# Kernel optimization log

Hardware: AMD Instinct MI355X
Metric: run time of the kernel (lower is better)

The kernel has to match this reference:

```python
import jax, jax.numpy as jnp
import numpy as np

EMBED = 1024

def setup_inputs() -> dict:
    key = jax.random.key(0)
    ks = jax.random.split(key, 7)
    s = 1.0 / np.sqrt(EMBED)
    x = jax.random.normal(ks[0], (8, 2048, EMBED), dtype=jnp.float32)
    Wk = jax.random.uniform(ks[1], (EMBED, EMBED), jnp.float32, -s, s)
    bk = jax.random.uniform(ks[2], (EMBED,), jnp.float32, -s, s)
    Wq = jax.random.uniform(ks[3], (EMBED, EMBED), jnp.float32, -s, s)
    bq = jax.random.uniform(ks[4], (EMBED,), jnp.float32, -s, s)
    Wv = jax.random.uniform(ks[5], (EMBED, EMBED), jnp.float32, -s, s)
    bv = jax.random.uniform(ks[6], (EMBED,), jnp.float32, -s, s)
    return {"x": x, "Wq": Wq, "bq": bq, "Wk": Wk, "bk": bk, "Wv": Wv, "bv": bv}

def reference(x, Wq, bq, Wk, bk, Wv, bv):
    # Linear projections (PyTorch Linear: y = x @ W^T + b; W here stored as [in, out] = W^T)
    Q = x @ Wq + bq          # [b, s, d]
    K = x @ Wk + bk
    V = x @ Wv + bv
    scale = 1.0 / jnp.sqrt(jnp.asarray(x.shape[-1], x.dtype))
    scores = jnp.einsum('bqd,bkd->bqk', Q, K) * scale  # [b, s, s]
    attn = jax.nn.softmax(scores, axis=-1)
    return jnp.einsum('bqk,bkd->bqd', attn, V)
```

## Files before the change

kernel.cpp:

```cpp
#include <hip/hip_runtime.h>

typedef __attribute__((ext_vector_type(4))) float f32x4;
typedef __attribute__((ext_vector_type(8))) short bf16x8;
typedef __attribute__((ext_vector_type(4))) unsigned short u16x4;

static __device__ __forceinline__ unsigned short f2bf(float f) {
    union { float f; unsigned int u; } a; a.f = f;
    unsigned int u = a.u;
    unsigned int r = (u + 0x7FFFu + ((u >> 16) & 1u)) >> 16;
    return (unsigned short)r;
}
static __device__ __forceinline__ float bf2f(unsigned short h) {
    union { unsigned int u; float f; } a; a.u = ((unsigned int)h) << 16;
    return a.f;
}
static __device__ __forceinline__ unsigned lds_off(const void* p) {
    return (unsigned)(unsigned long long)(const __attribute__((address_space(3))) void*)p;
}

__global__ __launch_bounds__(256) void cvt_f32_bf16(const float* __restrict__ in,
                                                    unsigned short* __restrict__ out) {
    long long i = ((long long)blockIdx.x * 256 + threadIdx.x) * 4;
    float4 f = *(const float4*)(in + i);
    u16x4 u;
    u[0] = f2bf(f.x); u[1] = f2bf(f.y); u[2] = f2bf(f.z); u[3] = f2bf(f.w);
    *(u16x4*)(out + i) = u;
}

__global__ __launch_bounds__(256) void transpose_w(const float* __restrict__ W0,
                                                   const float* __restrict__ W1,
                                                   const float* __restrict__ W2,
                                                   unsigned short* __restrict__ Wt) {
    __shared__ float t[32][33];
    int mat = blockIdx.z;
    const float* W = (mat == 0) ? W0 : (mat == 1) ? W1 : W2;
    unsigned short* out = Wt + (long long)mat * 1024 * 1024;
    int n0 = blockIdx.x * 32, k0 = blockIdx.y * 32;
    int tx = threadIdx.x, ty = threadIdx.y;
#pragma unroll
    for (int q = 0; q < 4; ++q)
        t[ty + 8 * q][tx] = W[(long long)(k0 + ty + 8 * q) * 1024 + n0 + tx];
    __syncthreads();
#pragma unroll
    for (int q = 0; q < 4; ++q)
        out[(long long)(n0 + ty + 8 * q) * 1024 + k0 + tx] = f2bf(t[tx][ty + 8 * q]);
}

#define GBM 256
#define GBN 256

template<int OUT_MODE, int BIAS_MODE>
__global__ __launch_bounds__(512, 2) void gemmcv(
    const unsigned short* __restrict__ A, int lda, long long strideA,
    const unsigned short* __restrict__ B, int ldb, long long strideB,
    void* __restrict__ Cv, int ldc, long long strideC,
    const float* __restrict__ bias, int K, float scale)
{
    __shared__ __align__(16) char lds[131072];

    const int gx = gridDim.x, gy = gridDim.y;
    int lin = blockIdx.x + gx * (blockIdx.y + gy * blockIdx.z);
    const int nwg = gx * gy * gridDim.z;
    const int qch = nwg >> 3;
    int swz = (lin & 7) * qch + (lin >> 3);
    const int bx = swz % gx; int t2 = swz / gx;
    const int by = t2 % gy;  const int bz = t2 / gy;

    const unsigned short* Ag = A + (long long)bz * strideA;
    const unsigned short* Bg = B + (long long)bz * strideB;
    const int m0 = by * GBM, n0 = bx * GBN;

    const int tid  = threadIdx.x;
    const int lane = tid & 63, w = tid >> 6;
    const int wm = w >> 2, wn = w & 3;
    const int l15 = lane & 15, l4 = lane >> 4;

    const int sr = lane >> 3;
    const int ss = (lane & 7) ^ sr;
    const unsigned short* Asrc = Ag + (long long)(m0 + w * 8 + sr) * lda + ss * 8;
    const unsigned short* Bsrc = Bg + (long long)(n0 + w * 8 + sr) * ldb + ss * 8;

    f32x4 acc[8][4] = {};

    auto stageA = [&](int p, int kt, int h) {
#pragma unroll
        for (int i = 0; i < 2; ++i)
            __builtin_amdgcn_global_load_lds(
                (const __attribute__((address_space(1))) void*)(Asrc + (long long)(h * 128 + i * 64) * lda + kt),
                (__attribute__((address_space(3))) void*)(lds + p * 32768 + (h * 128 + i * 64 + w * 8) * 128), 16, 0, 0);
    };
    auto stageB = [&](int p, int kt, int h) {
#pragma unroll
        for (int i = 0; i < 2; ++i)
            __builtin_amdgcn_global_load_lds(
                (const __attribute__((address_space(1))) void*)(Bsrc + (long long)(h * 128 + i * 64) * ldb + kt),
                (__attribute__((address_space(3))) void*)(lds + 65536 + p * 32768 + (h * 128 + i * 64 + w * 8) * 128), 16, 0, 0);
    };

    const unsigned ldsb = lds_off(lds);
    const unsigned as0  = (unsigned)(((l4    ) ^ (l15 & 7)) * 16);
    const unsigned as1  = (unsigned)(((l4 + 4) ^ (l15 & 7)) * 16);
    const unsigned aRow = (unsigned)((wm * 128 + l15) * 128);
    const unsigned bRow = (unsigned)((wn * 64 + l15) * 128);

    bf16x8 aA[4], aB[4], aC[4], aD[4], bA[4], bB[4];
    auto readA = [&](bf16x8 (&af)[4], int p, int mh, int ks) {
        unsigned base = ldsb + (unsigned)(p * 32768) + aRow + (unsigned)(mh * 8192) + (ks ? as1 : as0);
#pragma unroll
        for (int fi = 0; fi < 4; ++fi) {
            unsigned off = base + (unsigned)(fi * 2048);
            asm volatile("ds_read_b128 %0, %1" : "=v"(af[fi]) : "v"(off));
        }
    };
    auto readB = [&](bf16x8 (&bf)[4], int p, int ks) {
        unsigned base = ldsb + 65536u + (unsigned)(p * 32768) + bRow + (ks ? as1 : as0);
#pragma unroll
        for (int nj = 0; nj < 4; ++nj) {
            unsigned off = base + (unsigned)(nj * 2048);
            asm volatile("ds_read_b128 %0, %1" : "=v"(bf[nj]) : "v"(off));
        }
    };
    auto mfma16 = [&](int mh, bf16x8 (&af)[4], bf16x8 (&bf)[4]) {
#pragma unroll
        for (int fi = 0; fi < 4; ++fi)
#pragma unroll
            for (int nj = 0; nj < 4; ++nj)
                acc[mh * 4 + fi][nj] = __builtin_amdgcn_mfma_f32_16x16x32_bf16(
                    af[fi], bf[nj], acc[mh * 4 + fi][nj], 0, 0, 0);
    };

#define VMCNT4 asm volatile("s_waitcnt vmcnt(4)" ::: "memory")
#define VMCNT2 asm volatile("s_waitcnt vmcnt(2)" ::: "memory")
#define VMCNT0 asm volatile("s_waitcnt vmcnt(0)" ::: "memory")
#define LGKM8  asm volatile("s_waitcnt lgkmcnt(8)" ::: "memory")
#define LGKM4  asm volatile("s_waitcnt lgkmcnt(4)" ::: "memory")
#define LGKM0  asm volatile("s_waitcnt lgkmcnt(0)" ::: "memory")
#define SCHED0 __builtin_amdgcn_sched_barrier(0)
#define BARR   __builtin_amdgcn_s_barrier()
#define PRIO1  __builtin_amdgcn_s_setprio(1)
#define PRIO0  __builtin_amdgcn_s_setprio(0)

    const int NT = K >> 6;
    stageB(0, 0, 0); stageB(0, 0, 1); stageA(0, 0, 0); stageA(0, 0, 1);

    for (int t = 0; t < NT; ++t) {
        const int p = t & 1, q = p ^ 1;
        const int kt1 = (t + 1) << 6;
        const bool s1 = (t + 1) < NT;
        VMCNT2; BARR; SCHED0;
        if (s1) { stageB(q, kt1, 0); stageB(q, kt1, 1); }
        readA(aA, p, 0, 0); readB(bA, p, 0);
        readA(aC, p, 0, 1); readB(bB, p, 1);
        LGKM8; SCHED0; PRIO1; mfma16(0, aA, bA); PRIO0;
        if (s1) { VMCNT4; } else { VMCNT0; }
        BARR; SCHED0;
        if (s1) { stageA(q, kt1, 0); stageA(q, kt1, 1); }
        readA(aB, p, 1, 0); readA(aD, p, 1, 1);
        LGKM8; SCHED0; PRIO1; mfma16(0, aC, bB); PRIO0;
        LGKM4; SCHED0; PRIO1; mfma16(1, aB, bA); PRIO0;
        LGKM0; SCHED0; PRIO1; mfma16(1, aD, bB); PRIO0;
    }

    const float* bias_v = bias;
    asm volatile("" : "+s"(bias_v));
    unsigned short* Cb = (unsigned short*)Cv;
    float* Cf = (float*)Cv;
    long long cbase = (long long)bz * strideC;
#pragma unroll
    for (int mh = 0; mh < 2; ++mh)
#pragma unroll
    for (int fi = 0; fi < 4; ++fi) {
#pragma unroll
        for (int nj = 0; nj < 4; ++nj) {
            int n = n0 + wn * 64 + nj * 16 + l15;
            float bn = (BIAS_MODE == 1) ? bias_v[n] : 0.0f;
#pragma unroll
            for (int r = 0; r < 4; ++r) {
                int m = m0 + wm * 128 + mh * 64 + fi * 16 + l4 * 4 + r;
                float v = acc[mh * 4 + fi][nj][r] * scale + bn;
                if (BIAS_MODE == 2) v += bias_v[m];
                long long idx = cbase + (long long)m * ldc + n;
                if (OUT_MODE == 0) Cb[idx] = f2bf(v);
                else               Cf[idx] = v;
            }
        }
    }
}

__global__ __launch_bounds__(256) void softmax_rows_bf16(unsigned short* __restrict__ S) {
    int row  = blockIdx.x * 4 + (threadIdx.x >> 6);
    int lane = threadIdx.x & 63;
    unsigned short* Srow = S + (long long)row * 2048;
    float v[32];
    float mx = -1e30f;
#pragma unroll
    for (int j = 0; j < 4; ++j) {
        bf16x8 h = *(const bf16x8*)(Srow + j * 512 + lane * 8);
#pragma unroll
        for (int e = 0; e < 8; ++e) {
            float f = bf2f((unsigned short)h[e]);
            v[j * 8 + e] = f;
            mx = fmaxf(mx, f);
        }
    }
#pragma unroll
    for (int o = 32; o; o >>= 1) mx = fmaxf(mx, __shfl_xor(mx, o));
    float sum = 0.0f;
#pragma unroll
    for (int e = 0; e < 32; ++e) {
        v[e] = __expf(v[e] - mx);
        sum += v[e];
    }
#pragma unroll
    for (int o = 32; o; o >>= 1) sum += __shfl_xor(sum, o);
    float inv = 1.0f / sum;
#pragma unroll
    for (int j = 0; j < 4; ++j) {
        bf16x8 h;
#pragma unroll
        for (int e = 0; e < 8; ++e) h[e] = (short)f2bf(v[j * 8 + e] * inv);
        *(bf16x8*)(Srow + j * 512 + lane * 8) = h;
    }
}

extern "C" void kernel_launch(void* const* d_in, const int* in_sizes, int n_in,
                              void* d_out, int out_size, void* d_ws, size_t ws_size,
                              hipStream_t stream) {
    (void)in_sizes; (void)n_in; (void)out_size; (void)ws_size;
    const float* x  = (const float*)d_in[0];
    const float* Wq = (const float*)d_in[1];
    const float* bq = (const float*)d_in[2];
    const float* Wk = (const float*)d_in[3];
    const float* bk = (const float*)d_in[4];
    const float* Wv = (const float*)d_in[5];
    const float* bv = (const float*)d_in[6];

    char* ws = (char*)d_ws;
    unsigned short* Wt  = (unsigned short*)ws;
    unsigned short* Qb  = (unsigned short*)(ws + 6291456);
    unsigned short* Kb  = (unsigned short*)(ws + 39845888);
    unsigned short* Vt  = (unsigned short*)(ws + 73400320);
    unsigned short* xb  = (unsigned short*)(ws + 106954752);
    unsigned short* Sb  = (unsigned short*)(ws + 106954752);

    cvt_f32_bf16<<<dim3(16384), dim3(256), 0, stream>>>(x, xb);
    transpose_w<<<dim3(32, 32, 3), dim3(32, 8), 0, stream>>>(Wq, Wk, Wv, Wt);

    gemmcv<0, 1><<<dim3(4, 64, 1), dim3(512), 0, stream>>>(
        xb, 1024, 0, Wt, 1024, 0, Qb, 1024, 0, bq, 1024, 1.0f);
    gemmcv<0, 1><<<dim3(4, 64, 1), dim3(512), 0, stream>>>(
        xb, 1024, 0, Wt + 1048576, 1024, 0, Kb, 1024, 0, bk, 1024, 1.0f);
    gemmcv<0, 2><<<dim3(64, 4, 1), dim3(512), 0, stream>>>(
        Wt + 2097152, 1024, 0, xb, 1024, 0, Vt, 16384, 0, bv, 1024, 1.0f);

    gemmcv<0, 0><<<dim3(8, 8, 8), dim3(512), 0, stream>>>(
        Qb, 1024, 2097152LL, Kb, 1024, 2097152LL,
        Sb, 2048, 4194304LL, nullptr, 1024, 0.03125f);

    softmax_rows_bf16<<<dim3(4096), dim3(256), 0, stream>>>(Sb);

    gemmcv<1, 0><<<dim3(4, 8, 8), dim3(512), 0, stream>>>(
        Sb, 2048, 4194304LL,
        Vt, 16384, 2048LL,
        d_out, 1024, 2097152LL, nullptr, 2048, 1.0f);
}
```

Baseline: 278.0 us.

## Stage A tile through registers instead of direct global-to-LDS loads

The A operand is now loaded from global memory into registers early in each iteration and written to the alternate LDS buffer late, while B keeps using direct global_load_lds. This removes the mid-iteration barrier and vmcnt wait that gated the A staging, leaving one barrier per K step. In exchange it uses extra VGPRs for the staged A fragments and adds explicit ds_write traffic that competes with the ds_reads used by the MFMAs.

After: 300.8 us. +8.2%, slower.

```diff
diff --git a/kernel.cpp b/kernel.cpp
--- a/kernel.cpp
+++ b/kernel.cpp
@@ -50,7 +50,7 @@
 #define GBN 256
 
 template<int OUT_MODE, int BIAS_MODE>
-__global__ __launch_bounds__(512, 2) void gemmcv(
+__global__ __launch_bounds__(512, 2) void gemmt14(
     const unsigned short* __restrict__ A, int lda, long long strideA,
     const unsigned short* __restrict__ B, int ldb, long long strideB,
     void* __restrict__ Cv, int ldc, long long strideC,
@@ -80,15 +80,17 @@
     const unsigned short* Asrc = Ag + (long long)(m0 + w * 8 + sr) * lda + ss * 8;
     const unsigned short* Bsrc = Bg + (long long)(n0 + w * 8 + sr) * ldb + ss * 8;
 
+    const unsigned short* AsrcJ[4];
+    unsigned awr[4];
+#pragma unroll
+    for (int j = 0; j < 4; ++j) {
+        AsrcJ[j] = Asrc + (long long)(j * 64) * lda;
+        awr[j]   = (unsigned)((j * 64 + w * 8 + sr) * 128 + (lane & 7) * 16);
+    }
+    bf16x8 areg[4];
+
     f32x4 acc[8][4] = {};
 
-    auto stageA = [&](int p, int kt, int h) {
-#pragma unroll
-        for (int i = 0; i < 2; ++i)
-            __builtin_amdgcn_global_load_lds(
-                (const __attribute__((address_space(1))) void*)(Asrc + (long long)(h * 128 + i * 64) * lda + kt),
-                (__attribute__((address_space(3))) void*)(lds + p * 32768 + (h * 128 + i * 64 + w * 8) * 128), 16, 0, 0);
-    };
     auto stageB = [&](int p, int kt, int h) {
 #pragma unroll
         for (int i = 0; i < 2; ++i)
@@ -129,8 +131,6 @@
                     af[fi], bf[nj], acc[mh * 4 + fi][nj], 0, 0, 0);
     };
 
-#define VMCNT4 asm volatile("s_waitcnt vmcnt(4)" ::: "memory")
-#define VMCNT2 asm volatile("s_waitcnt vmcnt(2)" ::: "memory")
 #define VMCNT0 asm volatile("s_waitcnt vmcnt(0)" ::: "memory")
 #define LGKM8  asm volatile("s_waitcnt lgkmcnt(8)" ::: "memory")
 #define LGKM4  asm volatile("s_waitcnt lgkmcnt(4)" ::: "memory")
@@ -141,24 +141,35 @@
 #define PRIO0  __builtin_amdgcn_s_setprio(0)
 
     const int NT = K >> 6;
-    stageB(0, 0, 0); stageB(0, 0, 1); stageA(0, 0, 0); stageA(0, 0, 1);
+#pragma unroll
+    for (int j = 0; j < 4; ++j) areg[j] = *(const bf16x8*)(AsrcJ[j]);
+    stageB(0, 0, 0); stageB(0, 0, 1);
+#pragma unroll
+    for (int j = 0; j < 4; ++j) *(bf16x8*)(&lds[awr[j]]) = areg[j];
+    LGKM0; VMCNT0; BARR; SCHED0;
 
     for (int t = 0; t < NT; ++t) {
         const int p = t & 1, q = p ^ 1;
         const int kt1 = (t + 1) << 6;
         const bool s1 = (t + 1) < NT;
-        VMCNT2; BARR; SCHED0;
-        if (s1) { stageB(q, kt1, 0); stageB(q, kt1, 1); }
+        if (s1) {
+#pragma unroll
+            for (int j = 0; j < 4; ++j) areg[j] = *(const bf16x8*)(AsrcJ[j] + kt1);
+            stageB(q, kt1, 0); stageB(q, kt1, 1);
+        }
         readA(aA, p, 0, 0); readB(bA, p, 0);
         readA(aC, p, 0, 1); readB(bB, p, 1);
         LGKM8; SCHED0; PRIO1; mfma16(0, aA, bA); PRIO0;
-        if (s1) { VMCNT4; } else { VMCNT0; }
-        BARR; SCHED0;
-        if (s1) { stageA(q, kt1, 0); stageA(q, kt1, 1); }
         readA(aB, p, 1, 0); readA(aD, p, 1, 1);
         LGKM8; SCHED0; PRIO1; mfma16(0, aC, bB); PRIO0;
         LGKM4; SCHED0; PRIO1; mfma16(1, aB, bA); PRIO0;
+        if (s1) {
+#pragma unroll
+            for (int j = 0; j < 4; ++j) *(bf16x8*)(&lds[(q * 32768) + awr[j]]) = areg[j];
+        }
         LGKM0; SCHED0; PRIO1; mfma16(1, aD, bB); PRIO0;
+        if (s1) { VMCNT0; }
+        BARR; SCHED0;
     }
 
     const float* bias_v = bias;
@@ -246,20 +257,20 @@
     cvt_f32_bf16<<<dim3(16384), dim3(256), 0, stream>>>(x, xb);
     transpose_w<<<dim3(32, 32, 3), dim3(32, 8), 0, stream>>>(Wq, Wk, Wv, Wt);
 
-    gemmcv<0, 1><<<dim3(4, 64, 1), dim3(512), 0, stream>>>(
+    gemmt14<0, 1><<<dim3(4, 64, 1), dim3(512), 0, stream>>>(
         xb, 1024, 0, Wt, 1024, 0, Qb, 1024, 0, bq, 1024, 1.0f);
-    gemmcv<0, 1><<<dim3(4, 64, 1), dim3(512), 0, stream>>>(
+    gemmt14<0, 1><<<dim3(4, 64, 1), dim3(512), 0, stream>>>(
         xb, 1024, 0, Wt + 1048576, 1024, 0, Kb, 1024, 0, bk, 1024, 1.0f);
-    gemmcv<0, 2><<<dim3(64, 4, 1), dim3(512), 0, stream>>>(
+    gemmt14<0, 2><<<dim3(64, 4, 1), dim3(512), 0, stream>>>(
         Wt + 2097152, 1024, 0, xb, 1024, 0, Vt, 16384, 0, bv, 1024, 1.0f);
 
-    gemmcv<0, 0><<<dim3(8, 8, 8), dim3(512), 0, stream>>>(
+    gemmt14<0, 0><<<dim3(8, 8, 8), dim3(512), 0, stream>>>(
         Qb, 1024, 2097152LL, Kb, 1024, 2097152LL,
         Sb, 2048, 4194304LL, nullptr, 1024, 0.03125f);
 
     softmax_rows_bf16<<<dim3(4096), dim3(256), 0, stream>>>(Sb);
 
-    gemmcv<1, 0><<<dim3(4, 8, 8), dim3(512), 0, stream>>>(
+    gemmt14<1, 0><<<dim3(4, 8, 8), dim3(512), 0, stream>>>(
         Sb, 2048, 4194304LL,
         Vt, 16384, 2048LL,
         d_out, 1024, 2097152LL, nullptr, 2048, 1.0f);
```

## Store Q and K in FP8 and compute attention scores with FP8 MFMA

Applied to the files above, without the earlier changes.

The Q and K projection GEMMs now write FP8 e4m3 outputs pre-scaled by 16 instead of bf16. A new FP8 GEMM kernel computes QK^T with 16x16x32 fp8 MFMA over 128-wide K tiles, with new LDS swizzling and a reworked read/compute schedule, then rescales the result into bf16 scores. This halves Q/K memory traffic and raises matrix throughput for the score GEMM, at the cost of lower precision in the attention scores.

New measurement: 270.9 us. 1.03x faster.

```diff
diff --git a/kernel.cpp b/kernel.cpp
--- a/kernel.cpp
+++ b/kernel.cpp
@@ -1,4 +1,5 @@
 #include <hip/hip_runtime.h>
+#include <hip/hip_fp8.h>
 
 typedef __attribute__((ext_vector_type(4))) float f32x4;
 typedef __attribute__((ext_vector_type(8))) short bf16x8;
@@ -13,6 +14,10 @@
 static __device__ __forceinline__ float bf2f(unsigned short h) {
     union { unsigned int u; float f; } a; a.u = ((unsigned int)h) << 16;
     return a.f;
+}
+static __device__ __forceinline__ unsigned char f2fp8(float f) {
+    __hip_fp8_e4m3 h(f);
+    return *reinterpret_cast<const unsigned char*>(&h);
 }
 static __device__ __forceinline__ unsigned lds_off(const void* p) {
     return (unsigned)(unsigned long long)(const __attribute__((address_space(3))) void*)p;
@@ -46,6 +51,18 @@
         out[(long long)(n0 + ty + 8 * q) * 1024 + k0 + tx] = f2bf(t[tx][ty + 8 * q]);
 }
 
+#define SCHED0 __builtin_amdgcn_sched_barrier(0)
+#define BARR   __builtin_amdgcn_s_barrier()
+#define PRIO1  __builtin_amdgcn_s_setprio(1)
+#define PRIO0  __builtin_amdgcn_s_setprio(0)
+#define VMCNT4 asm volatile("s_waitcnt vmcnt(4)" ::: "memory")
+#define VMCNT2 asm volatile("s_waitcnt vmcnt(2)" ::: "memory")
+#define VMCNT0 asm volatile("s_waitcnt vmcnt(0)" ::: "memory")
+#define LGKM12 asm volatile("s_waitcnt lgkmcnt(12)" ::: "memory")
+#define LGKM8  asm volatile("s_waitcnt lgkmcnt(8)" ::: "memory")
+#define LGKM4  asm volatile("s_waitcnt lgkmcnt(4)" ::: "memory")
+#define LGKM0  asm volatile("s_waitcnt lgkmcnt(0)" ::: "memory")
+
 #define GBM 256
 #define GBN 256
 
@@ -128,17 +145,6 @@
                 acc[mh * 4 + fi][nj] = __builtin_amdgcn_mfma_f32_16x16x32_bf16(
                     af[fi], bf[nj], acc[mh * 4 + fi][nj], 0, 0, 0);
     };
-
-#define VMCNT4 asm volatile("s_waitcnt vmcnt(4)" ::: "memory")
-#define VMCNT2 asm volatile("s_waitcnt vmcnt(2)" ::: "memory")
-#define VMCNT0 asm volatile("s_waitcnt vmcnt(0)" ::: "memory")
-#define LGKM8  asm volatile("s_waitcnt lgkmcnt(8)" ::: "memory")
-#define LGKM4  asm volatile("s_waitcnt lgkmcnt(4)" ::: "memory")
-#define LGKM0  asm volatile("s_waitcnt lgkmcnt(0)" ::: "memory")
-#define SCHED0 __builtin_amdgcn_sched_barrier(0)
-#define BARR   __builtin_amdgcn_s_barrier()
-#define PRIO1  __builtin_amdgcn_s_setprio(1)
-#define PRIO0  __builtin_amdgcn_s_setprio(0)
 
     const int NT = K >> 6;
     stageB(0, 0, 0); stageB(0, 0, 1); stageA(0, 0, 0); stageA(0, 0, 1);
@@ -164,6 +170,7 @@
     const float* bias_v = bias;
     asm volatile("" : "+s"(bias_v));
     unsigned short* Cb = (unsigned short*)Cv;
+    unsigned char*  C8 = (unsigned char*)Cv;
     float* Cf = (float*)Cv;
     long long cbase = (long long)bz * strideC;
 #pragma unroll
@@ -180,8 +187,136 @@
                 float v = acc[mh * 4 + fi][nj][r] * scale + bn;
                 if (BIAS_MODE == 2) v += bias_v[m];
                 long long idx = cbase + (long long)m * ldc + n;
-                if (OUT_MODE == 0) Cb[idx] = f2bf(v);
-                else               Cf[idx] = v;
+                if (OUT_MODE == 0)      Cb[idx] = f2bf(v);
+                else if (OUT_MODE == 1) Cf[idx] = v;
+                else                    C8[idx] = f2fp8(v * 16.0f);
+            }
+        }
+    }
+}
+
+__global__ __launch_bounds__(512, 2) void gemmf8(
+    const unsigned char* __restrict__ A, int lda, long long strideA,
+    const unsigned char* __restrict__ B, int ldb, long long strideB,
+    unsigned short* __restrict__ C, int ldc, long long strideC,
+    int K, float scale)
+{
+    __shared__ __align__(16) char lds[131072];
+
+    const int gx = gridDim.x, gy = gridDim.y;
+    int lin = blockIdx.x + gx * (blockIdx.y + gy * blockIdx.z);
+    const int nwg = gx * gy * gridDim.z;
+    const int qch = nwg >> 3;
+    int swz = (lin & 7) * qch + (lin >> 3);
+    const int bx = swz % gx; int t2 = swz / gx;
+    const int by = t2 % gy;  const int bz = t2 / gy;
+
+    const unsigned char* Ag = A + (long long)bz * strideA;
+    const unsigned char* Bg = B + (long long)bz * strideB;
+    const int m0 = by * GBM, n0 = bx * GBN;
+
+    const int tid  = threadIdx.x;
+    const int lane = tid & 63, w = tid >> 6;
+    const int wm = w >> 2, wn = w & 3;
+    const int l15 = lane & 15, l4 = lane >> 4;
+
+    const int sr = lane >> 3;
+    const int c7 = lane & 7;
+    const int ss8 = (((((c7 >> 1) ^ (sr & 3)) << 1) | ((c7 & 1) ^ ((lane >> 5) & 1)))) * 16;
+    const unsigned char* Asrc = Ag + (long long)(m0 + w * 8 + sr) * lda + ss8;
+    const unsigned char* Bsrc = Bg + (long long)(n0 + w * 8 + sr) * ldb + ss8;
+
+    f32x4 acc[8][4] = {};
+
+    auto stageA = [&](int p, int kt, int h) {
+#pragma unroll
+        for (int i = 0; i < 2; ++i)
+            __builtin_amdgcn_global_load_lds(
+                (const __attribute__((address_space(1))) void*)(Asrc + (long long)(h * 128 + i * 64) * lda + kt),
+                (__attribute__((address_space(3))) void*)(lds + p * 32768 + (h * 128 + i * 64 + w * 8) * 128), 16, 0, 0);
+    };
+    auto stageB = [&](int p, int kt, int h) {
+#pragma unroll
+        for (int i = 0; i < 2; ++i)
+            __builtin_amdgcn_global_load_lds(
+                (const __attribute__((address_space(1))) void*)(Bsrc + (long long)(h * 128 + i * 64) * ldb + kt),
+                (__attribute__((address_space(3))) void*)(lds + 65536 + p * 32768 + (h * 128 + i * 64 + w * 8) * 128), 16, 0, 0);
+    };
+
+    const unsigned ldsb  = lds_off(lds);
+    const unsigned kbase = (unsigned)((l4 << 3) ^ (((l15 >> 2) & 1) << 4));
+    unsigned kk[4];
+#pragma unroll
+    for (int ks = 0; ks < 4; ++ks) kk[ks] = (unsigned)((ks ^ (l15 & 3)) << 5) + kbase;
+    const unsigned aRow = (unsigned)((wm * 128 + l15) * 128);
+    const unsigned bRow = (unsigned)((wn * 64 + l15) * 128) + 65536u;
+
+    long a0[4][4], a1[4][4], bb[4][4];
+    auto readA = [&](long (&af)[4], int p, int mh, int ks) {
+        unsigned base = ldsb + (unsigned)(p * 32768) + aRow + (unsigned)(mh * 8192) + kk[ks];
+#pragma unroll
+        for (int fi = 0; fi < 4; ++fi) {
+            unsigned off = base + (unsigned)(fi * 2048);
+            asm volatile("ds_read_b64 %0, %1" : "=v"(af[fi]) : "v"(off));
+        }
+    };
+    auto readB = [&](long (&bf)[4], int p, int ks) {
+        unsigned base = ldsb + (unsigned)(p * 32768) + bRow + kk[ks];
+#pragma unroll
+        for (int nj = 0; nj < 4; ++nj) {
+            unsigned off = base + (unsigned)(nj * 2048);
+            asm volatile("ds_read_b64 %0, %1" : "=v"(bf[nj]) : "v"(off));
+        }
+    };
+    auto mf = [&](int mh, long (&af)[4], long (&bf)[4]) {
+#pragma unroll
+        for (int fi = 0; fi < 4; ++fi)
+#pragma unroll
+            for (int nj = 0; nj < 4; ++nj)
+                acc[mh * 4 + fi][nj] = __builtin_amdgcn_mfma_f32_16x16x32_fp8_fp8(
+                    af[fi], bf[nj], acc[mh * 4 + fi][nj], 0, 0, 0);
+    };
+
+    const int NT = K >> 7;
+    stageB(0, 0, 0); stageB(0, 0, 1); stageA(0, 0, 0); stageA(0, 0, 1);
+
+    for (int t = 0; t < NT; ++t) {
+        const int p = t & 1, q = p ^ 1;
+        const int kt1 = (t + 1) << 7;
+        const bool s1 = (t + 1) < NT;
+        VMCNT2; BARR; SCHED0;
+        if (s1) { stageB(q, kt1, 0); stageB(q, kt1, 1); }
+        readA(a0[0], p, 0, 0); readB(bb[0], p, 0);
+        readA(a0[1], p, 0, 1); readB(bb[1], p, 1);
+        LGKM8; SCHED0; PRIO1; mf(0, a0[0], bb[0]); PRIO0;
+        readA(a0[2], p, 0, 2); readB(bb[2], p, 2);
+        LGKM8; SCHED0; PRIO1; mf(0, a0[1], bb[1]); PRIO0;
+        if (s1) { VMCNT4; } else { VMCNT0; }
+        BARR; SCHED0;
+        if (s1) { stageA(q, kt1, 0); stageA(q, kt1, 1); }
+        readA(a0[3], p, 0, 3); readB(bb[3], p, 3);
+        LGKM8; SCHED0; PRIO1; mf(0, a0[2], bb[2]); PRIO0;
+        readA(a1[0], p, 1, 0); readA(a1[1], p, 1, 1);
+        LGKM8; SCHED0; PRIO1; mf(0, a0[3], bb[3]); PRIO0;
+        readA(a1[2], p, 1, 2); readA(a1[3], p, 1, 3);
+        LGKM12; SCHED0; PRIO1; mf(1, a1[0], bb[0]); PRIO0;
+        LGKM8;  SCHED0; PRIO1; mf(1, a1[1], bb[1]); PRIO0;
+        LGKM4;  SCHED0; PRIO1; mf(1, a1[2], bb[2]); PRIO0;
+        LGKM0;  SCHED0; PRIO1; mf(1, a1[3], bb[3]); PRIO0;
+    }
+
+    long long cbase = (long long)bz * strideC;
+#pragma unroll
+    for (int mh = 0; mh < 2; ++mh)
+#pragma unroll
+    for (int fi = 0; fi < 4; ++fi) {
+#pragma unroll
+        for (int nj = 0; nj < 4; ++nj) {
+            int n = n0 + wn * 64 + nj * 16 + l15;
+#pragma unroll
+            for (int r = 0; r < 4; ++r) {
+                int m = m0 + wm * 128 + mh * 64 + fi * 16 + l4 * 4 + r;
+                C[cbase + (long long)m * ldc + n] = f2bf(acc[mh * 4 + fi][nj][r] * scale);
             }
         }
     }
@@ -237,25 +372,25 @@
 
     char* ws = (char*)d_ws;
     unsigned short* Wt  = (unsigned short*)ws;
-    unsigned short* Qb  = (unsigned short*)(ws + 6291456);
-    unsigned short* Kb  = (unsigned short*)(ws + 39845888);
-    unsigned short* Vt  = (unsigned short*)(ws + 73400320);
-    unsigned short* xb  = (unsigned short*)(ws + 106954752);
-    unsigned short* Sb  = (unsigned short*)(ws + 106954752);
+    unsigned char*  Qb8 = (unsigned char*) (ws + 6291456);
+    unsigned char*  Kb8 = (unsigned char*) (ws + 23068672);
+    unsigned short* Vt  = (unsigned short*)(ws + 39845888);
+    unsigned short* xb  = (unsigned short*)(ws + 73400320);
+    unsigned short* Sb  = (unsigned short*)(ws + 73400320);
 
     cvt_f32_bf16<<<dim3(16384), dim3(256), 0, stream>>>(x, xb);
     transpose_w<<<dim3(32, 32, 3), dim3(32, 8), 0, stream>>>(Wq, Wk, Wv, Wt);
 
-    gemmcv<0, 1><<<dim3(4, 64, 1), dim3(512), 0, stream>>>(
-        xb, 1024, 0, Wt, 1024, 0, Qb, 1024, 0, bq, 1024, 1.0f);
-    gemmcv<0, 1><<<dim3(4, 64, 1), dim3(512), 0, stream>>>(
-        xb, 1024, 0, Wt + 1048576, 1024, 0, Kb, 1024, 0, bk, 1024, 1.0f);
+    gemmcv<2, 1><<<dim3(4, 64, 1), dim3(512), 0, stream>>>(
+        xb, 1024, 0, Wt, 1024, 0, Qb8, 1024, 0, bq, 1024, 1.0f);
+    gemmcv<2, 1><<<dim3(4, 64, 1), dim3(512), 0, stream>>>(
+        xb, 1024, 0, Wt + 1048576, 1024, 0, Kb8, 1024, 0, bk, 1024, 1.0f);
     gemmcv<0, 2><<<dim3(64, 4, 1), dim3(512), 0, stream>>>(
         Wt + 2097152, 1024, 0, xb, 1024, 0, Vt, 16384, 0, bv, 1024, 1.0f);
 
-    gemmcv<0, 0><<<dim3(8, 8, 8), dim3(512), 0, stream>>>(
-        Qb, 1024, 2097152LL, Kb, 1024, 2097152LL,
-        Sb, 2048, 4194304LL, nullptr, 1024, 0.03125f);
+    gemmf8<<<dim3(8, 8, 8), dim3(512), 0, stream>>>(
+        Qb8, 1024, 2097152LL, Kb8, 1024, 2097152LL,
+        Sb, 2048, 4194304LL, 1024, 1.0f / 8192.0f);
 
     softmax_rows_bf16<<<dim3(4096), dim3(256), 0, stream>>>(Sb);
 
```
